# Optimization experiments

Measured on AMD Instinct MI355X. Metric: run time of the kernel, lower is better.

## Reference

```python
import jax, jax.numpy as jnp
import numpy as np

N = 100000
E = 1200000
D = 64
EPS = 1e-5  # BatchNorm1d default eps


def setup_inputs() -> dict:
    key = jax.random.key(0)
    ks = jax.random.split(key, 5)
    x = jax.random.normal(ks[0], (N, D), dtype=jnp.float32)
    edge_index = jax.random.randint(ks[1], (2, E), 0, N, dtype=jnp.int32)
    W1 = jax.random.normal(ks[2], (D, D), dtype=jnp.float32) * (1.0 / np.sqrt(D))
    W2 = jax.random.normal(ks[3], (D, D), dtype=jnp.float32) * (1.0 / np.sqrt(D))
    return {
        'x': x,
        'edge_index': edge_index,
        'W1': W1,
        'b1': jnp.zeros((D,), jnp.float32),
        'gamma1': jnp.ones((D,), jnp.float32),
        'beta1': jnp.zeros((D,), jnp.float32),
        'W2': W2,
        'b2': jnp.zeros((D,), jnp.float32),
        'gamma2': jnp.ones((D,), jnp.float32),
        'beta2': jnp.zeros((D,), jnp.float32),
    }


def gcn_conv(x, src, dst, W, b):
    # GCNConv: xw = x @ W; add self-loops; symmetric deg^{-1/2} normalization;
    # scatter-add aggregation over incoming edges; + bias.
    xw = x @ W  # [N, out]
    # degree including self-loop (edge weight 1)
    deg = jnp.zeros((x.shape[0],), x.dtype).at[dst].add(1.0) + 1.0  # [N]
    dinv = jax.lax.rsqrt(deg)
    norm = dinv[src] * dinv[dst]  # [E]
    agg = jnp.zeros_like(xw).at[dst].add(norm[:, None] * xw[src])
    agg = agg + (dinv * dinv)[:, None] * xw  # self-loop term: deg^{-1} * xw
    return agg + b


def batchnorm(x, gamma, beta):
    # training-mode BatchNorm1d over node dimension (biased variance)
    mu = x.mean(axis=0)
    var = x.var(axis=0)
    return gamma * (x - mu) * jax.lax.rsqrt(var + EPS) + beta


def reference(x, edge_index, W1, b1, gamma1, beta1, W2, b2, gamma2, beta2):
    src, dst = edge_index[0], edge_index[1]
    h = gcn_conv(x, src, dst, W1, b1)
    h = jax.nn.leaky_relu(batchnorm(h, gamma1, beta1), 0.01)
    # dropout p=0.0 -> identity
    h = gcn_conv(h, src, dst, W2, b2)
    h = jax.nn.leaky_relu(batchnorm(h, gamma2, beta2), 0.01)
    return h
```

## Files before the change

kernel.cpp:

```cpp
#include <hip/hip_runtime.h>
#include <hip/hip_bf16.h>

#define NN 100000
#define NE 1200000
#define DD 64
#define EPS 1e-5f

#define NB 196
#define GEMM_BLOCKS ((NN + 63) / 64)
#define HIST_BLOCKS 256
#define PART_BLOCKS 256
#define EPH ((NE + HIST_BLOCKS - 1) / HIST_BLOCKS)
#define EPB ((NE + PART_BLOCKS - 1) / PART_BLOCKS)

typedef short bf16x8_t __attribute__((ext_vector_type(8)));
typedef float f32x4_t  __attribute__((ext_vector_type(4)));

__device__ __forceinline__ short f2bf(float f) {
    __hip_bfloat16 h = __float2bfloat16(f);
    return reinterpret_cast<short&>(h);
}
__device__ __forceinline__ float bf2f(short s) {
    return __uint_as_float(((unsigned)(unsigned short)s) << 16);
}

template <bool BN>
__device__ __forceinline__ void gemm_tile(const float* __restrict__ X,
                                          const float* __restrict__ W,
                                          __hip_bfloat16* __restrict__ XWh,
                                          const float* __restrict__ stats,
                                          const float* __restrict__ gamma,
                                          const float* __restrict__ beta,
                                          int blk) {
    __shared__ __align__(16) short xhi[64 * 72];
    __shared__ __align__(16) short xlo[64 * 72];
    __shared__ __align__(16) short wt[64 * 72];
    __shared__ float sc_s[64], sh_s[64];
    int t = threadIdx.x;
    int row0 = blk * 64;

    if (BN) {
        if (t < 64) {
            const float inv_n = 1.0f / (float)NN;
            float mu  = stats[t] * inv_n;
            float var = stats[64 + t] * inv_n - mu * mu;
            float sc  = gamma[t] * rsqrtf(var + EPS);
            sc_s[t] = sc;
            sh_s[t] = beta[t] - sc * mu;
        }
        __syncthreads();
    }

    for (int i = t; i < 64 * 64; i += 256) {
        int k = i >> 6, n = i & 63;
        wt[n * 72 + k] = f2bf(W[k * 64 + n]);
    }

    for (int it = 0; it < 4; ++it) {
        int i = it * 256 + t;
        int r = i >> 4, c4 = i & 15;
        int grow = row0 + r;
        float4 v = make_float4(0.f, 0.f, 0.f, 0.f);
        if (grow < NN) v = ((const float4*)(X + (size_t)grow * 64))[c4];
        if (BN) {
            float4 s4 = ((const float4*)sc_s)[c4];
            float4 h4 = ((const float4*)sh_s)[c4];
            v.x = s4.x * v.x + h4.x; v.x = fmaxf(v.x, 0.01f * v.x);
            v.y = s4.y * v.y + h4.y; v.y = fmaxf(v.y, 0.01f * v.y);
            v.z = s4.z * v.z + h4.z; v.z = fmaxf(v.z, 0.01f * v.z);
            v.w = s4.w * v.w + h4.w; v.w = fmaxf(v.w, 0.01f * v.w);
        }
        short h0 = f2bf(v.x), h1 = f2bf(v.y), h2 = f2bf(v.z), h3 = f2bf(v.w);
        short l0 = f2bf(v.x - bf2f(h0)), l1 = f2bf(v.y - bf2f(h1));
        short l2 = f2bf(v.z - bf2f(h2)), l3 = f2bf(v.w - bf2f(h3));
        int base = r * 72 + c4 * 4;
        *(short4*)&xhi[base] = make_short4(h0, h1, h2, h3);
        *(short4*)&xlo[base] = make_short4(l0, l1, l2, l3);
    }
    __syncthreads();

    int w = t >> 6;
    int l = t & 63;
    int fr = l & 15;
    int fq = l >> 4;
    int abase = (w * 16 + fr) * 72 + fq * 8;

    bf16x8_t ahi0 = *(const bf16x8_t*)&xhi[abase];
    bf16x8_t ahi1 = *(const bf16x8_t*)&xhi[abase + 32];
    bf16x8_t alo0 = *(const bf16x8_t*)&xlo[abase];
    bf16x8_t alo1 = *(const bf16x8_t*)&xlo[abase + 32];

    f32x4_t acc[4];
#pragma unroll
    for (int c = 0; c < 4; ++c) acc[c] = (f32x4_t){0.f, 0.f, 0.f, 0.f};

#pragma unroll
    for (int c = 0; c < 4; ++c) {
        int bbase = (c * 16 + fr) * 72 + fq * 8;
        bf16x8_t b0 = *(const bf16x8_t*)&wt[bbase];
        bf16x8_t b1 = *(const bf16x8_t*)&wt[bbase + 32];
        acc[c] = __builtin_amdgcn_mfma_f32_16x16x32_bf16(ahi0, b0, acc[c], 0, 0, 0);
        acc[c] = __builtin_amdgcn_mfma_f32_16x16x32_bf16(alo0, b0, acc[c], 0, 0, 0);
        acc[c] = __builtin_amdgcn_mfma_f32_16x16x32_bf16(ahi1, b1, acc[c], 0, 0, 0);
        acc[c] = __builtin_amdgcn_mfma_f32_16x16x32_bf16(alo1, b1, acc[c], 0, 0, 0);
    }

#pragma unroll
    for (int c = 0; c < 4; ++c) {
#pragma unroll
        for (int i = 0; i < 4; ++i) {
            int grow = row0 + w * 16 + fq * 4 + i;
            if (grow < NN)
                XWh[(size_t)grow * 64 + c * 16 + fr] = __float2bfloat16(acc[c][i]);
        }
    }
}

__global__ __launch_bounds__(256) void k_histscan(const int* __restrict__ dst,
                                                  int* __restrict__ cnt196,
                                                  int* __restrict__ done,
                                                  int* __restrict__ bo,
                                                  int* __restrict__ cur) {
    __shared__ int h[NB];
    __shared__ int s[256];
    __shared__ int lastflag;
    for (int t = threadIdx.x; t < NB; t += 256) h[t] = 0;
    __syncthreads();
    int s0 = blockIdx.x * EPH;
    int s1 = s0 + EPH; if (s1 > NE) s1 = NE;
    for (int i = s0 + threadIdx.x; i < s1; i += 256)
        atomicAdd(&h[dst[i] >> 9], 1);
    __syncthreads();
    for (int t = threadIdx.x; t < NB; t += 256)
        if (h[t]) atomicAdd(&cnt196[t], h[t]);
    __threadfence();
    if (threadIdx.x == 0)
        lastflag = (atomicAdd(done, 1) == HIST_BLOCKS - 1);
    __syncthreads();
    if (lastflag) {
        int t = threadIdx.x;
        int v = (t < NB) ? atomicAdd(&cnt196[t], 0) : 0;
        s[t] = v;
        __syncthreads();
        for (int o = 1; o < 256; o <<= 1) {
            int u = (t >= o) ? s[t - o] : 0;
            __syncthreads();
            s[t] += u;
            __syncthreads();
        }
        if (t < NB) {
            int ex = s[t] - v;
            bo[t] = ex;
            cur[t] = ex;
        }
        if (t == 0) bo[NB] = NE;
    }
}

__global__ __launch_bounds__(256) void k_pg(const float* __restrict__ X,
                                            const float* __restrict__ W,
                                            __hip_bfloat16* __restrict__ XWh,
                                            const int* __restrict__ src,
                                            const int* __restrict__ dst,
                                            int* __restrict__ cur,
                                            int* __restrict__ ebuf) {
    if (blockIdx.x < PART_BLOCKS) {
        __shared__ int h[NB];
        for (int t = threadIdx.x; t < NB; t += 256) h[t] = 0;
        __syncthreads();
        int s0 = blockIdx.x * EPB;
        int s1 = s0 + EPB; if (s1 > NE) s1 = NE;
        for (int i = s0 + threadIdx.x; i < s1; i += 256)
            atomicAdd(&h[dst[i] >> 9], 1);
        __syncthreads();
        for (int t = threadIdx.x; t < NB; t += 256) {
            int c = h[t];
            h[t] = c ? atomicAdd(&cur[t], c) : 0;
        }
        __syncthreads();
        for (int i = s0 + threadIdx.x; i < s1; i += 256) {
            int d = dst[i];
            int p = atomicAdd(&h[d >> 9], 1);
            ebuf[p] = src[i] | ((d & 511) << 17);
        }
    } else {
        gemm_tile<false>(X, W, XWh, nullptr, nullptr, nullptr,
                         (int)blockIdx.x - PART_BLOCKS);
    }
}

__global__ __launch_bounds__(256) void k_gemm2(const float* __restrict__ X,
                                               const float* __restrict__ W,
                                               __hip_bfloat16* __restrict__ XWh,
                                               const float* __restrict__ stats,
                                               const float* __restrict__ gamma,
                                               const float* __restrict__ beta) {
    gemm_tile<true>(X, W, XWh, stats, gamma, beta, blockIdx.x);
}

__global__ __launch_bounds__(512) void k_bucket(const int* __restrict__ ebuf,
                                                const int* __restrict__ bo,
                                                int* __restrict__ off,
                                                float* __restrict__ dinv,
                                                int* __restrict__ esrc) {
    __shared__ int s[512];
    int b = blockIdx.x, t = threadIdx.x;
    int base = b << 9;
    int e0 = bo[b], e1 = bo[b + 1];
    s[t] = 0;
    __syncthreads();
    for (int e = e0 + t; e < e1; e += 512)
        atomicAdd(&s[ebuf[e] >> 17], 1);
    __syncthreads();
    int deg = s[t];
    if (base + t < NN) dinv[base + t] = rsqrtf((float)deg + 1.0f);
    for (int o = 1; o < 512; o <<= 1) {
        int u = (t >= o) ? s[t - o] : 0;
        __syncthreads();
        s[t] += u;
        __syncthreads();
    }
    int gstart = e0 + s[t] - deg;
    if (base + t < NN) off[base + t] = gstart;
    if (b == NB - 1 && t == 0) off[NN] = NE;
    __syncthreads();
    s[t] = gstart;
    __syncthreads();
    for (int e = e0 + t; e < e1; e += 512) {
        int v = ebuf[e];
        int p = atomicAdd(&s[v >> 17], 1);
        esrc[p] = v & 0x1FFFF;
    }
}

__device__ __forceinline__ void bf16x8d(uint4 u, float* f) {
    f[0] = __uint_as_float(u.x << 16);
    f[1] = __uint_as_float(u.x & 0xFFFF0000u);
    f[2] = __uint_as_float(u.y << 16);
    f[3] = __uint_as_float(u.y & 0xFFFF0000u);
    f[4] = __uint_as_float(u.z << 16);
    f[5] = __uint_as_float(u.z & 0xFFFF0000u);
    f[6] = __uint_as_float(u.w << 16);
    f[7] = __uint_as_float(u.w & 0xFFFF0000u);
}

__global__ __launch_bounds__(256) void k_agg(const __hip_bfloat16* __restrict__ XWh,
                                             const int* __restrict__ off,
                                             const int* __restrict__ esrc,
                                             const float* __restrict__ dinv,
                                             float* __restrict__ out) {
    const uint4* __restrict__ XW4 = (const uint4*)XWh;
    int team = threadIdx.x >> 3;
    int sub  = threadIdx.x & 7;
    int node = blockIdx.x * 32 + team;

    float di = dinv[node];
    float a[8], b[8], r0[8], r1[8];
    uint4 us = XW4[(size_t)node * 8 + sub];
    bf16x8d(us, a);
#pragma unroll
    for (int i = 0; i < 8; ++i) { a[i] *= di; b[i] = 0.0f; }

    int e0 = off[node], e1 = off[node + 1];
    int e = e0;
    for (; e + 1 < e1; e += 2) {
        int s0 = esrc[e];
        int s1 = esrc[e + 1];
        float n0 = dinv[s0], n1 = dinv[s1];
        uint4 u0 = XW4[(size_t)s0 * 8 + sub];
        uint4 u1 = XW4[(size_t)s1 * 8 + sub];
        bf16x8d(u0, r0);
        bf16x8d(u1, r1);
#pragma unroll
        for (int i = 0; i < 8; ++i) a[i] += n0 * r0[i];
#pragma unroll
        for (int i = 0; i < 8; ++i) b[i] += n1 * r1[i];
    }
    if (e < e1) {
        int s0 = esrc[e];
        float n0 = dinv[s0];
        uint4 u0 = XW4[(size_t)s0 * 8 + sub];
        bf16x8d(u0, r0);
#pragma unroll
        for (int i = 0; i < 8; ++i) a[i] += n0 * r0[i];
    }
#pragma unroll
    for (int i = 0; i < 8; ++i) a[i] = (a[i] + b[i]) * di;

    float4* o4 = (float4*)out;
    o4[(size_t)node * 16 + sub * 2]     = make_float4(a[0], a[1], a[2], a[3]);
    o4[(size_t)node * 16 + sub * 2 + 1] = make_float4(a[4], a[5], a[6], a[7]);
}

__global__ __launch_bounds__(256) void k_stats(const float* __restrict__ X,
                                               float* __restrict__ stats, int n) {
    __shared__ float ls[4][64], lq[4][64];
    int lane = threadIdx.x & 63, rg = threadIdx.x >> 6;
    float s = 0.0f, sq = 0.0f;
    for (int r = blockIdx.x * 4 + rg; r < n; r += gridDim.x * 4) {
        float v = X[(size_t)r * 64 + lane];
        s += v; sq += v * v;
    }
    ls[rg][lane] = s; lq[rg][lane] = sq;
    __syncthreads();
    if (rg == 0) {
        s  = ls[0][lane] + ls[1][lane] + ls[2][lane] + ls[3][lane];
        sq = lq[0][lane] + lq[1][lane] + lq[2][lane] + lq[3][lane];
        atomicAdd(&stats[lane], s);
        atomicAdd(&stats[64 + lane], sq);
    }
}

__global__ __launch_bounds__(256) void k_bnact(const float* __restrict__ X,
                                               float* __restrict__ Y,
                                               const float* __restrict__ stats,
                                               const float* __restrict__ gamma,
                                               const float* __restrict__ beta,
                                               int n) {
    int lane = threadIdx.x & 63, rg = threadIdx.x >> 6;
    float inv_n = 1.0f / (float)n;
    float mu  = stats[lane] * inv_n;
    float var = stats[64 + lane] * inv_n - mu * mu;
    float sc  = gamma[lane] * rsqrtf(var + EPS);
    float sh  = beta[lane] - sc * mu;
    for (int r = blockIdx.x * 4 + rg; r < n; r += gridDim.x * 4) {
        float v = X[(size_t)r * 64 + lane];
        v = sc * v + sh;
        Y[(size_t)r * 64 + lane] = fmaxf(v, 0.01f * v);
    }
}

extern "C" void kernel_launch(void* const* d_in, const int* in_sizes, int n_in,
                              void* d_out, int out_size, void* d_ws, size_t ws_size,
                              hipStream_t stream) {
    const float* x   = (const float*)d_in[0];
    const int*   ei  = (const int*)d_in[1];
    const int*   src = ei;
    const int*   dst = ei + NE;
    const float* W1  = (const float*)d_in[2];
    const float* g1  = (const float*)d_in[4];
    const float* be1 = (const float*)d_in[5];
    const float* W2  = (const float*)d_in[6];
    const float* g2  = (const float*)d_in[8];
    const float* be2 = (const float*)d_in[9];
    float* out = (float*)d_out;

    char* ws = (char*)d_ws;
    size_t p = 0;
    auto alloc = [&](size_t bytes) {
        size_t o = p;
        p = (p + bytes + 255) & ~(size_t)255;
        return o;
    };
    int*   zeroed  = (int*)(ws + alloc(2304));
    int*   cnt196  = zeroed;
    float* stats   = (float*)(zeroed + 256);
    int*   done    = zeroed + 512;
    int*   bo      = (int*)(ws + alloc((size_t)(NB + 1) * 4));
    int*   cur     = (int*)(ws + alloc((size_t)NB * 4));
    int*   ebuf    = (int*)(ws + alloc((size_t)NE * 4));
    int*   esrc    = (int*)(ws + alloc((size_t)NE * 4));
    int*   off     = (int*)(ws + alloc((size_t)(NN + 1) * 4));
    float* dinv    = (float*)(ws + alloc((size_t)NN * 4));
    __hip_bfloat16* Ah = (__hip_bfloat16*)(ws + alloc((size_t)NN * DD * 2));
    float* B       = (float*)(ws + alloc((size_t)NN * DD * 4));
    (void)ws_size; (void)in_sizes; (void)n_in; (void)out_size;

    hipMemsetAsync(zeroed, 0, 2304, stream);

    k_histscan<<<HIST_BLOCKS, 256, 0, stream>>>(dst, cnt196, done, bo, cur);
    k_pg<<<PART_BLOCKS + GEMM_BLOCKS, 256, 0, stream>>>(x, W1, Ah, src, dst, cur, ebuf);
    k_bucket<<<NB, 512, 0, stream>>>(ebuf, bo, off, dinv, esrc);

    k_agg<<<NN / 32, 256, 0, stream>>>(Ah, off, esrc, dinv, B);
    k_stats<<<512, 256, 0, stream>>>(B, stats, NN);

    k_gemm2<<<GEMM_BLOCKS, 256, 0, stream>>>(B, W2, Ah, stats, g1, be1);
    k_agg<<<NN / 32, 256, 0, stream>>>(Ah, off, esrc, dinv, B);
    k_stats<<<512, 256, 0, stream>>>(B, stats + 128, NN);
    k_bnact<<<1024, 256, 0, stream>>>(B, out, stats + 128, g2, be2, NN);
}
```

Measured before the change: 280.4 us.

## Store aggregation outputs in bf16 and drop split-precision MMA in second GEMM

The aggregation kernels now write their node features as bf16 instead of fp32. The stats, second-GEMM and BN/activation kernels read that bf16 buffer, which halves the intermediate memory traffic. The second GEMM drops the hi/lo split and its extra MFMAs, since its input is already bf16. Partition blocks are doubled. The trade-off is lower precision in the intermediate activations and BN statistics, which could affect accuracy tolerance.

Result: faster. 262.0 us (-6.6%).

```diff
diff --git a/kernel.cpp b/kernel.cpp
--- a/kernel.cpp
+++ b/kernel.cpp
@@ -9,7 +9,7 @@
 #define NB 196
 #define GEMM_BLOCKS ((NN + 63) / 64)
 #define HIST_BLOCKS 256
-#define PART_BLOCKS 256
+#define PART_BLOCKS 512
 #define EPH ((NE + HIST_BLOCKS - 1) / HIST_BLOCKS)
 #define EPB ((NE + PART_BLOCKS - 1) / PART_BLOCKS)
 
@@ -23,9 +23,13 @@
 __device__ __forceinline__ float bf2f(short s) {
     return __uint_as_float(((unsigned)(unsigned short)s) << 16);
 }
+__device__ __forceinline__ unsigned packbf(float f0, float f1) {
+    return ((unsigned)(unsigned short)f2bf(f0)) |
+           (((unsigned)(unsigned short)f2bf(f1)) << 16);
+}
 
 template <bool BN>
-__device__ __forceinline__ void gemm_tile(const float* __restrict__ X,
+__device__ __forceinline__ void gemm_tile(const void* __restrict__ Xv,
                                           const float* __restrict__ W,
                                           __hip_bfloat16* __restrict__ XWh,
                                           const float* __restrict__ stats,
@@ -56,26 +60,37 @@
         wt[n * 72 + k] = f2bf(W[k * 64 + n]);
     }
 
-    for (int it = 0; it < 4; ++it) {
-        int i = it * 256 + t;
-        int r = i >> 4, c4 = i & 15;
-        int grow = row0 + r;
-        float4 v = make_float4(0.f, 0.f, 0.f, 0.f);
-        if (grow < NN) v = ((const float4*)(X + (size_t)grow * 64))[c4];
-        if (BN) {
-            float4 s4 = ((const float4*)sc_s)[c4];
-            float4 h4 = ((const float4*)sh_s)[c4];
-            v.x = s4.x * v.x + h4.x; v.x = fmaxf(v.x, 0.01f * v.x);
-            v.y = s4.y * v.y + h4.y; v.y = fmaxf(v.y, 0.01f * v.y);
-            v.z = s4.z * v.z + h4.z; v.z = fmaxf(v.z, 0.01f * v.z);
-            v.w = s4.w * v.w + h4.w; v.w = fmaxf(v.w, 0.01f * v.w);
-        }
-        short h0 = f2bf(v.x), h1 = f2bf(v.y), h2 = f2bf(v.z), h3 = f2bf(v.w);
-        short l0 = f2bf(v.x - bf2f(h0)), l1 = f2bf(v.y - bf2f(h1));
-        short l2 = f2bf(v.z - bf2f(h2)), l3 = f2bf(v.w - bf2f(h3));
-        int base = r * 72 + c4 * 4;
-        *(short4*)&xhi[base] = make_short4(h0, h1, h2, h3);
-        *(short4*)&xlo[base] = make_short4(l0, l1, l2, l3);
+    if (BN) {
+        const unsigned* Xb = (const unsigned*)Xv;
+        for (int it = 0; it < 8; ++it) {
+            int i = it * 256 + t;
+            int r = i >> 5, cu = i & 31;
+            int grow = row0 + r;
+            float f0 = 0.f, f1 = 0.f;
+            if (grow < NN) {
+                unsigned u = Xb[(size_t)grow * 32 + cu];
+                f0 = __uint_as_float(u << 16);
+                f1 = __uint_as_float(u & 0xFFFF0000u);
+            }
+            f0 = sc_s[cu * 2] * f0 + sh_s[cu * 2];       f0 = fmaxf(f0, 0.01f * f0);
+            f1 = sc_s[cu * 2 + 1] * f1 + sh_s[cu * 2 + 1]; f1 = fmaxf(f1, 0.01f * f1);
+            *(unsigned*)&xhi[r * 72 + cu * 2] = packbf(f0, f1);
+        }
+    } else {
+        const float* Xf = (const float*)Xv;
+        for (int it = 0; it < 4; ++it) {
+            int i = it * 256 + t;
+            int r = i >> 4, c4 = i & 15;
+            int grow = row0 + r;
+            float4 v = make_float4(0.f, 0.f, 0.f, 0.f);
+            if (grow < NN) v = ((const float4*)(Xf + (size_t)grow * 64))[c4];
+            short h0 = f2bf(v.x), h1 = f2bf(v.y), h2 = f2bf(v.z), h3 = f2bf(v.w);
+            short l0 = f2bf(v.x - bf2f(h0)), l1 = f2bf(v.y - bf2f(h1));
+            short l2 = f2bf(v.z - bf2f(h2)), l3 = f2bf(v.w - bf2f(h3));
+            int base = r * 72 + c4 * 4;
+            *(short4*)&xhi[base] = make_short4(h0, h1, h2, h3);
+            *(short4*)&xlo[base] = make_short4(l0, l1, l2, l3);
+        }
     }
     __syncthreads();
 
@@ -87,8 +102,11 @@
 
     bf16x8_t ahi0 = *(const bf16x8_t*)&xhi[abase];
     bf16x8_t ahi1 = *(const bf16x8_t*)&xhi[abase + 32];
-    bf16x8_t alo0 = *(const bf16x8_t*)&xlo[abase];
-    bf16x8_t alo1 = *(const bf16x8_t*)&xlo[abase + 32];
+    bf16x8_t alo0, alo1;
+    if (!BN) {
+        alo0 = *(const bf16x8_t*)&xlo[abase];
+        alo1 = *(const bf16x8_t*)&xlo[abase + 32];
+    }
 
     f32x4_t acc[4];
 #pragma unroll
@@ -100,9 +118,11 @@
         bf16x8_t b0 = *(const bf16x8_t*)&wt[bbase];
         bf16x8_t b1 = *(const bf16x8_t*)&wt[bbase + 32];
         acc[c] = __builtin_amdgcn_mfma_f32_16x16x32_bf16(ahi0, b0, acc[c], 0, 0, 0);
-        acc[c] = __builtin_amdgcn_mfma_f32_16x16x32_bf16(alo0, b0, acc[c], 0, 0, 0);
         acc[c] = __builtin_amdgcn_mfma_f32_16x16x32_bf16(ahi1, b1, acc[c], 0, 0, 0);
-        acc[c] = __builtin_amdgcn_mfma_f32_16x16x32_bf16(alo1, b1, acc[c], 0, 0, 0);
+        if (!BN) {
+            acc[c] = __builtin_amdgcn_mfma_f32_16x16x32_bf16(alo0, b0, acc[c], 0, 0, 0);
+            acc[c] = __builtin_amdgcn_mfma_f32_16x16x32_bf16(alo1, b1, acc[c], 0, 0, 0);
+        }
     }
 
 #pragma unroll
@@ -189,7 +209,7 @@
     }
 }
 
-__global__ __launch_bounds__(256) void k_gemm2(const float* __restrict__ X,
+__global__ __launch_bounds__(256) void k_gemm2(const __hip_bfloat16* __restrict__ X,
                                                const float* __restrict__ W,
                                                __hip_bfloat16* __restrict__ XWh,
                                                const float* __restrict__ stats,
@@ -248,7 +268,7 @@
                                              const int* __restrict__ off,
                                              const int* __restrict__ esrc,
                                              const float* __restrict__ dinv,
-                                             float* __restrict__ out) {
+                                             __hip_bfloat16* __restrict__ outh) {
     const uint4* __restrict__ XW4 = (const uint4*)XWh;
     int team = threadIdx.x >> 3;
     int sub  = threadIdx.x & 7;
@@ -287,46 +307,71 @@
 #pragma unroll
     for (int i = 0; i < 8; ++i) a[i] = (a[i] + b[i]) * di;
 
-    float4* o4 = (float4*)out;
-    o4[(size_t)node * 16 + sub * 2]     = make_float4(a[0], a[1], a[2], a[3]);
-    o4[(size_t)node * 16 + sub * 2 + 1] = make_float4(a[4], a[5], a[6], a[7]);
-}
-
-__global__ __launch_bounds__(256) void k_stats(const float* __restrict__ X,
+    uint4 ob;
+    ob.x = packbf(a[0], a[1]);
+    ob.y = packbf(a[2], a[3]);
+    ob.z = packbf(a[4], a[5]);
+    ob.w = packbf(a[6], a[7]);
+    ((uint4*)outh)[(size_t)node * 8 + sub] = ob;
+}
+
+__global__ __launch_bounds__(256) void k_stats(const __hip_bfloat16* __restrict__ Xh,
                                                float* __restrict__ stats, int n) {
-    __shared__ float ls[4][64], lq[4][64];
-    int lane = threadIdx.x & 63, rg = threadIdx.x >> 6;
-    float s = 0.0f, sq = 0.0f;
-    for (int r = blockIdx.x * 4 + rg; r < n; r += gridDim.x * 4) {
-        float v = X[(size_t)r * 64 + lane];
-        s += v; sq += v * v;
-    }
-    ls[rg][lane] = s; lq[rg][lane] = sq;
-    __syncthreads();
-    if (rg == 0) {
-        s  = ls[0][lane] + ls[1][lane] + ls[2][lane] + ls[3][lane];
-        sq = lq[0][lane] + lq[1][lane] + lq[2][lane] + lq[3][lane];
-        atomicAdd(&stats[lane], s);
-        atomicAdd(&stats[64 + lane], sq);
-    }
-}
-
-__global__ __launch_bounds__(256) void k_bnact(const float* __restrict__ X,
+    __shared__ float ls[8][64], lq[8][64];
+    const unsigned* X = (const unsigned*)Xh;
+    int c  = threadIdx.x & 31;
+    int rg = threadIdx.x >> 5;
+    float s0 = 0.f, q0 = 0.f, s1 = 0.f, q1 = 0.f;
+    for (int r = blockIdx.x * 8 + rg; r < n; r += gridDim.x * 8) {
+        unsigned u = X[(size_t)r * 32 + c];
+        float f0 = __uint_as_float(u << 16);
+        float f1 = __uint_as_float(u & 0xFFFF0000u);
+        s0 += f0; q0 += f0 * f0;
+        s1 += f1; q1 += f1 * f1;
+    }
+    ls[rg][c * 2] = s0; ls[rg][c * 2 + 1] = s1;
+    lq[rg][c * 2] = q0; lq[rg][c * 2 + 1] = q1;
+    __syncthreads();
+    if (threadIdx.x < 64) {
+        int t = threadIdx.x;
+        float s = 0.f;
+#pragma unroll
+        for (int g = 0; g < 8; ++g) s += ls[g][t];
+        atomicAdd(&stats[t], s);
+    } else if (threadIdx.x < 128) {
+        int t = threadIdx.x - 64;
+        float q = 0.f;
+#pragma unroll
+        for (int g = 0; g < 8; ++g) q += lq[g][t];
+        atomicAdd(&stats[64 + t], q);
+    }
+}
+
+__global__ __launch_bounds__(256) void k_bnact(const __hip_bfloat16* __restrict__ Xh,
                                                float* __restrict__ Y,
                                                const float* __restrict__ stats,
                                                const float* __restrict__ gamma,
                                                const float* __restrict__ beta,
                                                int n) {
-    int lane = threadIdx.x & 63, rg = threadIdx.x >> 6;
+    const unsigned* X = (const unsigned*)Xh;
+    int c  = threadIdx.x & 31;
+    int rg = threadIdx.x >> 5;
     float inv_n = 1.0f / (float)n;
-    float mu  = stats[lane] * inv_n;
-    float var = stats[64 + lane] * inv_n - mu * mu;
-    float sc  = gamma[lane] * rsqrtf(var + EPS);
-    float sh  = beta[lane] - sc * mu;
-    for (int r = blockIdx.x * 4 + rg; r < n; r += gridDim.x * 4) {
-        float v = X[(size_t)r * 64 + lane];
-        v = sc * v + sh;
-        Y[(size_t)r * 64 + lane] = fmaxf(v, 0.01f * v);
+    float mu0  = stats[c * 2] * inv_n;
+    float mu1  = stats[c * 2 + 1] * inv_n;
+    float var0 = stats[64 + c * 2] * inv_n - mu0 * mu0;
+    float var1 = stats[64 + c * 2 + 1] * inv_n - mu1 * mu1;
+    float sc0  = gamma[c * 2] * rsqrtf(var0 + EPS);
+    float sc1  = gamma[c * 2 + 1] * rsqrtf(var1 + EPS);
+    float sh0  = beta[c * 2] - sc0 * mu0;
+    float sh1  = beta[c * 2 + 1] - sc1 * mu1;
+    for (int r = blockIdx.x * 8 + rg; r < n; r += gridDim.x * 8) {
+        unsigned u = X[(size_t)r * 32 + c];
+        float f0 = __uint_as_float(u << 16);
+        float f1 = __uint_as_float(u & 0xFFFF0000u);
+        f0 = sc0 * f0 + sh0; f0 = fmaxf(f0, 0.01f * f0);
+        f1 = sc1 * f1 + sh1; f1 = fmaxf(f1, 0.01f * f1);
+        ((float2*)Y)[(size_t)r * 32 + c] = make_float2(f0, f1);
     }
 }
 
@@ -363,7 +408,7 @@
     int*   off     = (int*)(ws + alloc((size_t)(NN + 1) * 4));
     float* dinv    = (float*)(ws + alloc((size_t)NN * 4));
     __hip_bfloat16* Ah = (__hip_bfloat16*)(ws + alloc((size_t)NN * DD * 2));
-    float* B       = (float*)(ws + alloc((size_t)NN * DD * 4));
+    __hip_bfloat16* Bh = (__hip_bfloat16*)(ws + alloc((size_t)NN * DD * 2));
     (void)ws_size; (void)in_sizes; (void)n_in; (void)out_size;
 
     hipMemsetAsync(zeroed, 0, 2304, stream);
@@ -372,11 +417,11 @@
     k_pg<<<PART_BLOCKS + GEMM_BLOCKS, 256, 0, stream>>>(x, W1, Ah, src, dst, cur, ebuf);
     k_bucket<<<NB, 512, 0, stream>>>(ebuf, bo, off, dinv, esrc);
 
-    k_agg<<<NN / 32, 256, 0, stream>>>(Ah, off, esrc, dinv, B);
-    k_stats<<<512, 256, 0, stream>>>(B, stats, NN);
-
-    k_gemm2<<<GEMM_BLOCKS, 256, 0, stream>>>(B, W2, Ah, stats, g1, be1);
-    k_agg<<<NN / 32, 256, 0, stream>>>(Ah, off, esrc, dinv, B);
-    k_stats<<<512, 256, 0, stream>>>(B, stats + 128, NN);
-    k_bnact<<<1024, 256, 0, stream>>>(B, out, stats + 128, g2, be2, NN);
-}
+    k_agg<<<NN / 32, 256, 0, stream>>>(Ah, off, esrc, dinv, Bh);
+    k_stats<<<512, 256, 0, stream>>>(Bh, stats, NN);
+
+    k_gemm2<<<GEMM_BLOCKS, 256, 0, stream>>>(Bh, W2, Ah, stats, g1, be1);
+    k_agg<<<NN / 32, 256, 0, stream>>>(Ah, off, esrc, dinv, Bh);
+    k_stats<<<512, 256, 0, stream>>>(Bh, stats + 128, NN);
+    k_bnact<<<1024, 256, 0, stream>>>(Bh, out, stats + 128, g2, be2, NN);
+}
```
